# Kernel tuning notes

Hardware: AMD Instinct MI355X
Metric: run time of the kernel (lower is better)

The kernel has to match this reference:

```python
import jax, jax.numpy as jnp
import numpy as np

L = 1024; B = 64; K = 5; C = 128; R = 32; E = 64
NL = 6; NV = 2; NF = NL - NV; NC = 4; POOL = 2


def conv1d(x, w, b, dil=1):
    # x: [B, Cin, L], w: [Cout, Cin, k] -> [B, Cout, L], 'same' padding
    y = jax.lax.conv_general_dilated(x, w, (1,), 'SAME', rhs_dilation=(dil,),
                                     dimension_numbers=('NCH', 'OIH', 'NCH'))
    return y + b[None, :, None]


def block(x, w1, b1, w2, b2, dil):
    h = jax.nn.relu(conv1d(x, w1, b1, dil))
    return jax.nn.relu(conv1d(h, w2, b2))


def setup_inputs() -> dict:
    key = jax.random.key(0)
    ks = iter(jax.random.split(key, 40))
    def p(shape, scale=0.05):
        return jax.random.normal(next(ks), shape, jnp.float32) * scale
    sig = jax.random.normal(next(ks), (B, L), jnp.float32)
    ids = jax.random.randint(next(ks), (B,), 0, NC).astype(jnp.float32)
    x = jnp.concatenate([sig, ids[:, None]], axis=1)  # [B, L+1], last col = combination id
    return dict(
        x=x,
        enc0_w1=p((C, 1, K)), enc0_b1=p((C,)), enc0_w2=p((R, C, 1)), enc0_b2=p((R,)),
        enc_w1=p((NL - 1, C, R, K)), enc_b1=p((NL - 1, C)),
        enc_w2=p((NL - 1, R, C, 1)), enc_b2=p((NL - 1, R)),
        comp_w=p((E, R * NL, 1)), comp_b=p((E,)),
        decf0_w1=p((C, E, K)), decf0_b1=p((C,)), decf0_w2=p((R, C, 1)), decf0_b2=p((R,)),
        decf_w1=p((NF - 1, C, R, K)), decf_b1=p((NF - 1, C)),
        decf_w2=p((NF - 1, R, C, 1)), decf_b2=p((NF - 1, R)),
        decv_w1=p((NC, NV, C, R, K)), decv_b1=p((NC, NV, C)),
        decv_w2=p((NC, NV, R, C, 1)), decv_b2=p((NC, NV, R)),
        decv_cw=p((NC, 1, R * NL, 1)), decv_cb=p((NC, 1)),
    )


def reference(x, enc0_w1, enc0_b1, enc0_w2, enc0_b2, enc_w1, enc_b1, enc_w2, enc_b2,
              comp_w, comp_b, decf0_w1, decf0_b1, decf0_w2, decf0_b2,
              decf_w1, decf_b1, decf_w2, decf_b2,
              decv_w1, decv_b1, decv_w2, decv_b2, decv_cw, decv_cb):
    ids = jax.lax.stop_gradient(x[:, L]).astype(jnp.int32)  # combination id per sample
    h = x[:, :L][:, None, :]  # [B, 1, L]
    # --- encoder: 6 dilated blocks, concat all features ---
    feats = []
    h = block(h, enc0_w1, enc0_b1, enc0_w2, enc0_b2, 1)
    feats.append(h)
    for j in range(1, NL):
        h = block(h, enc_w1[j - 1], enc_b1[j - 1], enc_w2[j - 1], enc_b2[j - 1], 2 ** j)
        feats.append(h)
    enc = conv1d(jnp.concatenate(feats, axis=1), comp_w, comp_b)  # [B, E, L]
    enc = enc.reshape(B, E, L // POOL, POOL).mean(-1)  # AvgPool1d(POOL)
    # nearest-neighbor interpolate back to L (exact integer upscale)
    h = jnp.repeat(enc, POOL, axis=-1)
    # --- fixed decoder blocks ---
    dec = []
    h = block(h, decf0_w1, decf0_b1, decf0_w2, decf0_b2, 2 ** (NL - 1))
    dec.append(h)
    for j in range(1, NF):
        h = block(h, decf_w1[j - 1], decf_b1[j - 1], decf_w2[j - 1], decf_b2[j - 1], 2 ** (NL - 1 - j))
        dec.append(h)
    # --- per-combination variable decoder (dense dispatch + mask select) ---
    y = jnp.zeros((B, 1, L), x.dtype)
    for c in range(NC):
        hc = h
        dc = list(dec)
        for j in range(NV):
            hc = block(hc, decv_w1[c, j], decv_b1[c, j], decv_w2[c, j], decv_b2[c, j], 2 ** (NV - 1 - j))
            dc.append(hc)
        out_c = conv1d(jnp.concatenate(dc, axis=1), decv_cw[c], decv_cb[c])  # [B, 1, L]
        y = y + jnp.where((ids == c)[:, None, None], out_c, 0.0)
    return y[:, 0, :]  # [B, L]
```

## Files before the change

### kernel.cpp

```cpp
#include <hip/hip_runtime.h>
#include <hip/hip_bf16.h>

typedef unsigned short u16;
typedef short s8v __attribute__((ext_vector_type(8)));
typedef float f4v __attribute__((ext_vector_type(4)));


struct Ptrs { const float* p[25]; };

enum : int { ACT_PLANE = 2359296 };

__host__ __device__ inline int w1_off16(int l) {
  if (l == 0) return 0;
  if (l <= 5) return 4096 + (l - 1) * 20480;
  if (l == 6) return 106496;
  if (l <= 9) return 147456 + (l - 7) * 20480;
  return 208896 + (l - 10) * 20480;
}

enum : int {
  OFF_W1H = 0,
  OFF_W1L = 186368,
  OFF_W2H = 372736,
  OFF_W2L = 409600,
  OFF_CWT = 446464,
  OFF_B1  = 458752,
  OFF_B2  = 461056,
  OFF_CB  = 461632,
  OFF_VCW = 461696,
  OFF_VCB = 462464,
  OFF_PACC = 524288,
  OFF_FACC = 2621440,
  OFF_ACT0 = 2752512,
  OFF_ACT1 = 5111808,
};

__device__ __host__ inline int w1_cin(int l) { return l == 0 ? 1 : (l == 6 ? 64 : 32); }

__device__ inline const float* w1_src(const Ptrs& in, int l) {
  if (l == 0) return in.p[1];
  if (l <= 5) return in.p[5] + (l - 1) * 20480;
  if (l == 6) return in.p[11];
  if (l <= 9) return in.p[15] + (l - 7) * 20480;
  return in.p[19] + (l - 10) * 20480;
}
__device__ inline const float* w2_src(const Ptrs& in, int l) {
  if (l == 0) return in.p[3];
  if (l <= 5) return in.p[7] + (l - 1) * 4096;
  if (l == 6) return in.p[13];
  if (l <= 9) return in.p[17] + (l - 7) * 4096;
  return in.p[21] + (l - 10) * 4096;
}
__device__ inline const float* b1_src(const Ptrs& in, int l) {
  if (l == 0) return in.p[2];
  if (l <= 5) return in.p[6] + (l - 1) * 128;
  if (l == 6) return in.p[12];
  if (l <= 9) return in.p[16] + (l - 7) * 128;
  return in.p[20] + (l - 10) * 128;
}
__device__ inline const float* b2_src(const Ptrs& in, int l) {
  if (l == 0) return in.p[4];
  if (l <= 5) return in.p[8] + (l - 1) * 32;
  if (l == 6) return in.p[14];
  if (l <= 9) return in.p[18] + (l - 7) * 32;
  return in.p[22] + (l - 10) * 32;
}

__device__ inline u16 f2b(float v) {
  unsigned b = __float_as_uint(v);
  b += 0x7FFFu + ((b >> 16) & 1u);
  return (u16)(b >> 16);
}
__device__ inline float b2fl(u16 h) { return __uint_as_float((unsigned)h << 16); }
__device__ inline void splitf(float v, u16& h, u16& l) {
  h = f2b(v);
  l = f2b(v - b2fl(h));
}

__global__ __launch_bounds__(256) void prep_k(Ptrs in, float* __restrict__ ws) {
  const int job = blockIdx.x;
  const int sl = blockIdx.y;
  const int t = threadIdx.x;
  u16* w1h = (u16*)(ws + OFF_W1H);
  u16* w1l = (u16*)(ws + OFF_W1L);
  u16* w2h = (u16*)(ws + OFF_W2H);
  u16* w2l = (u16*)(ws + OFF_W2L);
  u16* cwH = (u16*)(ws + OFF_CWT);
  u16* cwL = cwH + 12288;
  if (job == 0) {
    if (sl == 0) {
      const float* src = w1_src(in, 0);
      for (int i = t; i < 4096; i += 256) {
        const int co = i >> 5, q = i & 31;
        const float v = (q < 5) ? src[co * 5 + q] : 0.f;
        u16 hh, ll; splitf(v, hh, ll);
        w1h[i] = hh; w1l[i] = ll;
      }
    }
  } else if (job < 18) {
    const int cin = w1_cin(job);
    const int lc = (cin == 64) ? 6 : 5;
    const float* src = w1_src(in, job);
    u16* dh = w1h + w1_off16(job);
    u16* dl = w1l + w1_off16(job);
    const int n = 5 * 128 * cin;
    for (int i = t + sl * 256; i < n; i += 2048) {
      const int tap = i >> (7 + lc);
      const int co = (i >> lc) & 127;
      const int ci = i & (cin - 1);
      u16 hh, ll; splitf(src[(co * cin + ci) * 5 + tap], hh, ll);
      dh[i] = hh; dl[i] = ll;
    }
  } else if (job < 36) {
    const int l = job - 18;
    const float* src = w2_src(in, l);
    for (int i = t + sl * 256; i < 4096; i += 2048) {
      u16 hh, ll; splitf(src[i], hh, ll);
      w2h[l * 4096 + i] = hh; w2l[l * 4096 + i] = ll;
    }
  } else if (job == 36) {
    const float* src = in.p[9];
    for (int i = t + sl * 256; i < 12288; i += 2048) {
      u16 hh, ll; splitf(src[i], hh, ll);
      cwH[i] = hh; cwL[i] = ll;
    }
  } else if (job == 37) {
    if (sl == 0) {
      for (int i = t; i < 18 * 128; i += 256) {
        const int l = i >> 7, r = i & 127;
        ws[OFF_B1 + i] = b1_src(in, l)[r];
      }
      for (int i = t; i < 18 * 32; i += 256) {
        const int l = i >> 5, r = i & 31;
        ws[OFF_B2 + i] = b2_src(in, l)[r];
      }
      for (int i = t; i < 64; i += 256) ws[OFF_CB + i] = in.p[10][i];
      for (int i = t; i < 768; i += 256) ws[OFF_VCW + i] = in.p[23][i];
      for (int i = t; i < 4; i += 256) ws[OFF_VCB + i] = in.p[24][i];
    }
  } else {
    u16* A = (u16*)(ws + (job == 38 ? OFF_ACT0 : OFF_ACT1));
    const uint4 z = make_uint4(0, 0, 0, 0);
    for (int i = t; i < 8192; i += 256) {
      const int cid = sl * 8192 + i;
      const int p = cid >> 15;
      const int r = cid & 32767;
      const int b = r >> 9;
      const int r2 = r & 511;
      const int pc = r2 >> 2;
      const int slot = r2 & 3;
      const int col = (pc < 64) ? pc : (1024 + pc);
      *(uint4*)&A[p * ACT_PLANE + (b * 1152 + col) * 32 + slot * 8] = z;
    }
  }
}

template <int CIN, int S, bool VAR, int EPI>
__global__ __launch_bounds__(256, 4) void blk_k(
    const void* __restrict__ src,
    const u16* __restrict__ w1h, const u16* __restrict__ w1l,
    const u16* __restrict__ w2h, const u16* __restrict__ w2l,
    const float* __restrict__ b1f, const float* __restrict__ b2f,
    u16* __restrict__ outH, int dil,
    const float* __restrict__ x, int jvar, int jf,
    const u16* __restrict__ cwtbH, const u16* __restrict__ cwtbL,
    const float* __restrict__ cb, float* __restrict__ pacc,
    const float* __restrict__ vcw, const float* __restrict__ vcb,
    float* __restrict__ facc, float* __restrict__ fout) {
  constexpr int HS = 136;
  __shared__ __align__(16) u16 lds[2 * 64 * HS];
  u16* hH = lds;
  u16* hL = lds + 64 * HS;

  const int tid = threadIdx.x;
  const int lane = tid & 63;
  const int wid = __builtin_amdgcn_readfirstlane(tid >> 6);
  const int l15 = lane & 15;
  const int g = lane >> 4;
  const int col0 = blockIdx.x * 64;
  const int b = blockIdx.y;

  if (VAR) {
    int c = (int)x[b * 1025 + 1024];
    c = c < 0 ? 0 : (c > 3 ? 3 : c);
    c = __builtin_amdgcn_readfirstlane(c);
    const int lo_ = c * 2 + jvar;
    w1h += lo_ * 20480; w1l += lo_ * 20480;
    w2h += lo_ * 4096;  w2l += lo_ * 4096;
    b1f += lo_ * 128;   b2f += lo_ * 32;
  }

  const int co0 = wid * 32;
  const f4v zf = {0.f, 0.f, 0.f, 0.f};
  const s8v z8 = {0, 0, 0, 0, 0, 0, 0, 0};
  f4v acc[2][4];
#pragma unroll
  for (int rt = 0; rt < 2; ++rt)
#pragma unroll
    for (int ct = 0; ct < 4; ++ct) acc[rt][ct] = zf;

  if (S == 1) {
    const u16* aH = (const u16*)src;
    const int gbase = (b * 1152 + col0) * 32;
#pragma unroll
    for (int k = 0; k < 3; ++k) {
      const int c2 = tid + k * 256;
      const int q = c2 >> 2, slot = c2 & 3;
      const uint4 v = *(const uint4*)(aH + gbase + c2 * 8);
      *(uint4*)&lds[q * 32 + ((slot ^ (q & 3)) << 3)] = v;
    }
#pragma unroll
    for (int k = 0; k < 3; ++k) {
      const int c2 = tid + k * 256;
      const int q = c2 >> 2, slot = c2 & 3;
      const uint4 v = *(const uint4*)(aH + ACT_PLANE + gbase + c2 * 8);
      *(uint4*)&lds[6144 + q * 32 + ((slot ^ (q & 3)) << 3)] = v;
    }
    __syncthreads();

#pragma unroll
    for (int tap = 0; tap < 5; ++tap) {
      s8v ah[2], al[2];
#pragma unroll
      for (int rt = 0; rt < 2; ++rt) {
        const int row = co0 + rt * 16 + l15;
        ah[rt] = *(const s8v*)(w1h + (tap * 128 + row) * 32 + 8 * g);
        al[rt] = *(const s8v*)(w1l + (tap * 128 + row) * 32 + 8 * g);
      }
#pragma unroll
      for (int ct = 0; ct < 4; ++ct) {
        const int q = ct * 16 + l15 + (tap - 2) * dil + 64;
        const int off = q * 32 + ((g ^ (q & 3)) << 3);
        const s8v bh = *(const s8v*)&lds[off];
        const s8v bl = *(const s8v*)&lds[6144 + off];
#pragma unroll
        for (int rt = 0; rt < 2; ++rt) {
          acc[rt][ct] = __builtin_amdgcn_mfma_f32_16x16x32_bf16(ah[rt], bh, acc[rt][ct], 0, 0, 0);
          acc[rt][ct] = __builtin_amdgcn_mfma_f32_16x16x32_bf16(ah[rt], bl, acc[rt][ct], 0, 0, 0);
          acc[rt][ct] = __builtin_amdgcn_mfma_f32_16x16x32_bf16(al[rt], bh, acc[rt][ct], 0, 0, 0);
        }
      }
    }
    __syncthreads();
  } else if (S == 0) {
    s8v ah[2], al[2];
#pragma unroll
    for (int rt = 0; rt < 2; ++rt) {
      const int row = co0 + rt * 16 + l15;
      ah[rt] = *(const s8v*)(w1h + row * 32 + 8 * g);
      al[rt] = *(const s8v*)(w1l + row * 32 + 8 * g);
    }
    const float* xf = (const float*)src;
#pragma unroll
    for (int ct = 0; ct < 4; ++ct) {
      s8v bh = z8, bl = z8;
#pragma unroll
      for (int j = 0; j < 8; ++j) {
        const int q = 8 * g + j;
        const int m = col0 + ct * 16 + l15 + (q - 2);
        float v = (q < 5 && (unsigned)m < 1024u) ? xf[b * 1025 + m] : 0.f;
        u16 hh, ll; splitf(v, hh, ll);
        bh[j] = (short)hh; bl[j] = (short)ll;
      }
#pragma unroll
      for (int rt = 0; rt < 2; ++rt) {
        acc[rt][ct] = __builtin_amdgcn_mfma_f32_16x16x32_bf16(ah[rt], bh, acc[rt][ct], 0, 0, 0);
        acc[rt][ct] = __builtin_amdgcn_mfma_f32_16x16x32_bf16(ah[rt], bl, acc[rt][ct], 0, 0, 0);
        acc[rt][ct] = __builtin_amdgcn_mfma_f32_16x16x32_bf16(al[rt], bh, acc[rt][ct], 0, 0, 0);
      }
    }
  } else {
    const float* pc = (const float*)src;
#pragma unroll
    for (int tap = 0; tap < 5; ++tap) {
#pragma unroll
      for (int ch = 0; ch < 2; ++ch) {
        s8v ah[2], al[2];
#pragma unroll
        for (int rt = 0; rt < 2; ++rt) {
          const int row = co0 + rt * 16 + l15;
          ah[rt] = *(const s8v*)(w1h + (tap * 128 + row) * 64 + ch * 32 + 8 * g);
          al[rt] = *(const s8v*)(w1l + (tap * 128 + row) * 64 + ch * 32 + 8 * g);
        }
#pragma unroll
        for (int ct = 0; ct < 4; ++ct) {
          const int m = col0 + ct * 16 + l15 + (tap - 2) * dil;
          s8v bh = z8, bl = z8;
          if ((unsigned)m < 1024u) {
            const int pcol = m >> 1;
#pragma unroll
            for (int j = 0; j < 8; ++j) {
              const float v = pc[b * 32768 + (ch * 32 + 8 * g + j) * 512 + pcol];
              u16 hh, ll; splitf(v, hh, ll);
              bh[j] = (short)hh; bl[j] = (short)ll;
            }
          }
#pragma unroll
          for (int rt = 0; rt < 2; ++rt) {
            acc[rt][ct] = __builtin_amdgcn_mfma_f32_16x16x32_bf16(ah[rt], bh, acc[rt][ct], 0, 0, 0);
            acc[rt][ct] = __builtin_amdgcn_mfma_f32_16x16x32_bf16(ah[rt], bl, acc[rt][ct], 0, 0, 0);
            acc[rt][ct] = __builtin_amdgcn_mfma_f32_16x16x32_bf16(al[rt], bh, acc[rt][ct], 0, 0, 0);
          }
        }
      }
    }
  }

#pragma unroll
  for (int rt = 0; rt < 2; ++rt) {
#pragma unroll
    for (int ct = 0; ct < 4; ++ct) {
      const int colw = ct * 16 + l15;
      unsigned ph0 = 0, ph1 = 0, pl0 = 0, pl1 = 0;
#pragma unroll
      for (int reg = 0; reg < 4; ++reg) {
        const int c2 = co0 + rt * 16 + 4 * g + reg;
        const float hv = fmaxf(acc[rt][ct][reg] + b1f[c2], 0.f);
        u16 hh, ll; splitf(hv, hh, ll);
        if (reg == 0)      { ph0 = hh;                  pl0 = ll; }
        else if (reg == 1) { ph0 |= (unsigned)hh << 16; pl0 |= (unsigned)ll << 16; }
        else if (reg == 2) { ph1 = hh;                  pl1 = ll; }
        else               { ph1 |= (unsigned)hh << 16; pl1 |= (unsigned)ll << 16; }
      }
      const int base = colw * HS + co0 + rt * 16 + 4 * g;
      *(uint2*)&hH[base] = make_uint2(ph0, ph1);
      *(uint2*)&hL[base] = make_uint2(pl0, pl1);
    }
  }
  __syncthreads();

  f4v acc2[2];
  acc2[0] = zf; acc2[1] = zf;
  const int colw2 = wid * 16 + l15;
#pragma unroll
  for (int ks = 0; ks < 4; ++ks) {
    const int k0 = ks * 32 + 8 * g;
    const s8v bh = *(const s8v*)&hH[colw2 * HS + k0];
    const s8v bl = *(const s8v*)&hL[colw2 * HS + k0];
#pragma unroll
    for (int rt = 0; rt < 2; ++rt) {
      const int row = rt * 16 + l15;
      const s8v ah2 = *(const s8v*)(w2h + row * 128 + k0);
      const s8v al2 = *(const s8v*)(w2l + row * 128 + k0);
      acc2[rt] = __builtin_amdgcn_mfma_f32_16x16x32_bf16(ah2, bh, acc2[rt], 0, 0, 0);
      acc2[rt] = __builtin_amdgcn_mfma_f32_16x16x32_bf16(ah2, bl, acc2[rt], 0, 0, 0);
      acc2[rt] = __builtin_amdgcn_mfma_f32_16x16x32_bf16(al2, bh, acc2[rt], 0, 0, 0);
    }
  }

  u16* outL = outH + ACT_PLANE;
  float vv[8];
#pragma unroll
  for (int rt = 0; rt < 2; ++rt) {
    unsigned ph0 = 0, ph1 = 0, pl0 = 0, pl1 = 0;
#pragma unroll
    for (int reg = 0; reg < 4; ++reg) {
      const int r = rt * 16 + 4 * g + reg;
      const float v = fmaxf(acc2[rt][reg] + b2f[r], 0.f);
      vv[rt * 4 + reg] = v;
      u16 hh, ll; splitf(v, hh, ll);
      if (reg == 0)      { ph0 = hh;                  pl0 = ll; }
      else if (reg == 1) { ph0 |= (unsigned)hh << 16; pl0 |= (unsigned)ll << 16; }
      else if (reg == 2) { ph1 = hh;                  pl1 = ll; }
      else               { ph1 |= (unsigned)hh << 16; pl1 |= (unsigned)ll << 16; }
    }
    if (EPI != 5) {
      const int ob = (b * 1152 + 64 + col0 + colw2) * 32 + rt * 16 + 4 * g;
      *(uint2*)&outH[ob] = make_uint2(ph0, ph1);
      *(uint2*)&outL[ob] = make_uint2(pl0, pl1);
    }
  }
  __syncthreads();

  if (EPI <= 2) {
    u16* spH = lds;
    u16* spL = lds + 1280;
    float vx[8];
#pragma unroll
    for (int i = 0; i < 8; ++i) vx[i] = __shfl_xor(vv[i], 1);
    if (!(l15 & 1)) {
      const int pl = colw2 >> 1;
#pragma unroll
      for (int i = 0; i < 8; ++i) {
        const int rt = i >> 2, reg = i & 3;
        const int r = rt * 16 + 4 * g + reg;
        const float pv = 0.5f * (vv[i] + vx[i]);
        u16 hh, ll; splitf(pv, hh, ll);
        spH[pl * 40 + r] = hh; spL[pl * 40 + r] = ll;
      }
    }
    __syncthreads();
    const u16* cwH = cwtbH + jf * 32;
    const u16* cwL = cwtbL + jf * 32;
    const s8v aH = *(const s8v*)(cwH + (wid * 16 + l15) * 192 + 8 * g);
    const s8v aL = *(const s8v*)(cwL + (wid * 16 + l15) * 192 + 8 * g);
#pragma unroll
    for (int pt = 0; pt < 2; ++pt) {
      const s8v bH = *(const s8v*)(spH + (pt * 16 + l15) * 40 + 8 * g);
      const s8v bL = *(const s8v*)(spL + (pt * 16 + l15) * 40 + 8 * g);
      f4v p = zf;
      p = __builtin_amdgcn_mfma_f32_16x16x32_bf16(aH, bH, p, 0, 0, 0);
      p = __builtin_amdgcn_mfma_f32_16x16x32_bf16(aH, bL, p, 0, 0, 0);
      p = __builtin_amdgcn_mfma_f32_16x16x32_bf16(aL, bH, p, 0, 0, 0);
#pragma unroll
      for (int reg = 0; reg < 4; ++reg) {
        const int e = wid * 16 + 4 * g + reg;
        const int pg = (col0 >> 1) + pt * 16 + l15;
        float* dst = pacc + b * 32768 + e * 512 + pg;
        const float old = (EPI == 1) ? cb[e] : *dst;
        *dst = old + p[reg];
      }
    }
  } else {
    float* ft = (float*)lds;
#pragma unroll
    for (int i = 0; i < 8; ++i) {
      const int rt = i >> 2, reg = i & 3;
      const int r = rt * 16 + 4 * g + reg;
      ft[r * 64 + colw2] = vv[i];
    }
    __syncthreads();
    if (wid == 0) {
      int c = (int)x[b * 1025 + 1024];
      c = c < 0 ? 0 : (c > 3 ? 3 : c);
      c = __builtin_amdgcn_readfirstlane(c);
      const float* w = vcw + c * 192 + jf * 32;
      float a = 0.f;
#pragma unroll
      for (int r = 0; r < 32; ++r) a = fmaf(w[r], ft[r * 64 + lane], a);
      float* fd = facc + b * 1024 + col0 + lane;
      a += (EPI == 3) ? vcb[c] : *fd;
      if (EPI == 5) fout[b * 1024 + col0 + lane] = a;
      else          *fd = a;
    }
  }
}

extern "C" void kernel_launch(void* const* d_in, const int* in_sizes, int n_in,
                              void* d_out, int out_size, void* d_ws, size_t ws_size,
                              hipStream_t stream) {
  (void)in_sizes; (void)n_in; (void)out_size; (void)ws_size;
  Ptrs P;
  for (int i = 0; i < 25; ++i) P.p[i] = (const float*)d_in[i];
  const float* x = (const float*)d_in[0];
  float* ws = (float*)d_ws;
  float* pacc = ws + OFF_PACC;
  float* facc = ws + OFF_FACC;
  u16* A0 = (u16*)(ws + OFF_ACT0);
  u16* A1 = (u16*)(ws + OFF_ACT1);
  auto W1H = [&](int l) { return (const u16*)(ws + OFF_W1H) + w1_off16(l); };
  auto W1L = [&](int l) { return (const u16*)(ws + OFF_W1L) + w1_off16(l); };
  auto W2H = [&](int l) { return (const u16*)(ws + OFF_W2H) + l * 4096; };
  auto W2L = [&](int l) { return (const u16*)(ws + OFF_W2L) + l * 4096; };
  auto BB1 = [&](int l) { return (const float*)(ws + OFF_B1) + l * 128; };
  auto BB2 = [&](int l) { return (const float*)(ws + OFF_B2) + l * 32; };
  const u16* cwtbH = (const u16*)(ws + OFF_CWT);
  const u16* cwtbL = cwtbH + 12288;
  const float* cb = ws + OFF_CB;
  const float* vcw = ws + OFF_VCW;
  const float* vcb = ws + OFF_VCB;
  float* outp = (float*)d_out;

  prep_k<<<dim3(40, 8), dim3(256), 0, stream>>>(P, ws);

  const dim3 bg(16, 64), bt(256);

  blk_k<1, 0, false, 1><<<bg, bt, 0, stream>>>(x, W1H(0), W1L(0), W2H(0), W2L(0),
      BB1(0), BB2(0), A0, 1, x, 0, 0, cwtbH, cwtbL, cb, pacc, vcw, vcb, facc, outp);
  u16* cur = A0; u16* nxt = A1;
  for (int j = 1; j <= 5; ++j) {
    blk_k<32, 1, false, 2><<<bg, bt, 0, stream>>>(cur, W1H(j), W1L(j), W2H(j), W2L(j),
        BB1(j), BB2(j), nxt, 1 << j, x, 0, j, cwtbH, cwtbL, cb, pacc, vcw, vcb, facc, outp);
    u16* t = cur; cur = nxt; nxt = t;
  }
  blk_k<64, 2, false, 3><<<bg, bt, 0, stream>>>(pacc, W1H(6), W1L(6), W2H(6), W2L(6),
      BB1(6), BB2(6), A0, 32, x, 0, 0, cwtbH, cwtbL, cb, pacc, vcw, vcb, facc, outp);
  cur = A0; nxt = A1;
  for (int j = 1; j <= 3; ++j) {
    blk_k<32, 1, false, 4><<<bg, bt, 0, stream>>>(cur, W1H(6 + j), W1L(6 + j), W2H(6 + j),
        W2L(6 + j), BB1(6 + j), BB2(6 + j), nxt, 1 << (5 - j), x, 0, j,
        cwtbH, cwtbL, cb, pacc, vcw, vcb, facc, outp);
    u16* t = cur; cur = nxt; nxt = t;
  }
  blk_k<32, 1, true, 4><<<bg, bt, 0, stream>>>(cur, W1H(10), W1L(10), W2H(10), W2L(10),
      BB1(10), BB2(10), nxt, 2, x, 0, 4, cwtbH, cwtbL, cb, pacc, vcw, vcb, facc, outp);
  { u16* t = cur; cur = nxt; nxt = t; }
  blk_k<32, 1, true, 5><<<bg, bt, 0, stream>>>(cur, W1H(10), W1L(10), W2H(10), W2L(10),
      BB1(10), BB2(10), nxt, 1, x, 1, 5, cwtbH, cwtbL, cb, pacc, vcw, vcb, facc, outp);
}
```

Baseline: 400.5 us.

## Fuse all layer launches into one persistent cooperative kernel with grid syncs

Replaces the prep kernel and the twelve per-layer launches with a single cooperative mega-kernel. Blocks loop over 1024 tiles per layer and separate layers with grid.sync(). The goal is to remove launch gaps and tail effects between small kernels. In exchange, the epilogue selector becomes a runtime value instead of a template constant, which may add branching and register pressure. Grid-wide barriers can also cost more than kernel boundaries.

```diff
diff --git a/kernel.cpp b/kernel.cpp
--- a/kernel.cpp
+++ b/kernel.cpp
@@ -1,5 +1,8 @@
 #include <hip/hip_runtime.h>
 #include <hip/hip_bf16.h>
+#include <hip/hip_cooperative_groups.h>
+
+namespace cg = cooperative_groups;
 
 typedef unsigned short u16;
 typedef short s8v __attribute__((ext_vector_type(8)));
@@ -77,10 +80,7 @@
   l = f2b(v - b2fl(h));
 }
 
-__global__ __launch_bounds__(256) void prep_k(Ptrs in, float* __restrict__ ws) {
-  const int job = blockIdx.x;
-  const int sl = blockIdx.y;
-  const int t = threadIdx.x;
+__device__ void prep_body(int job, int sl, int t, const Ptrs& in, float* __restrict__ ws) {
   u16* w1h = (u16*)(ws + OFF_W1H);
   u16* w1l = (u16*)(ws + OFF_W1L);
   u16* w2h = (u16*)(ws + OFF_W2H);
@@ -155,20 +155,20 @@
   }
 }
 
-template <int CIN, int S, bool VAR, int EPI>
-__global__ __launch_bounds__(256, 4) void blk_k(
-    const void* __restrict__ src,
+template <int CIN, int S, bool VAR>
+__device__ void layer_body(
+    int tile, const void* __restrict__ src,
     const u16* __restrict__ w1h, const u16* __restrict__ w1l,
     const u16* __restrict__ w2h, const u16* __restrict__ w2l,
     const float* __restrict__ b1f, const float* __restrict__ b2f,
     u16* __restrict__ outH, int dil,
-    const float* __restrict__ x, int jvar, int jf,
+    const float* __restrict__ x, int jvar, int jf, int epi,
     const u16* __restrict__ cwtbH, const u16* __restrict__ cwtbL,
     const float* __restrict__ cb, float* __restrict__ pacc,
     const float* __restrict__ vcw, const float* __restrict__ vcb,
-    float* __restrict__ facc, float* __restrict__ fout) {
+    float* __restrict__ facc, float* __restrict__ fout,
+    u16* lds) {
   constexpr int HS = 136;
-  __shared__ __align__(16) u16 lds[2 * 64 * HS];
   u16* hH = lds;
   u16* hL = lds + 64 * HS;
 
@@ -177,8 +177,10 @@
   const int wid = __builtin_amdgcn_readfirstlane(tid >> 6);
   const int l15 = lane & 15;
   const int g = lane >> 4;
-  const int col0 = blockIdx.x * 64;
-  const int b = blockIdx.y;
+  const int col0 = (tile & 15) * 64;
+  const int b = tile >> 4;
+
+  __syncthreads();
 
   if (VAR) {
     int c = (int)x[b * 1025 + 1024];
@@ -364,7 +366,7 @@
       else if (reg == 2) { ph1 = hh;                  pl1 = ll; }
       else               { ph1 |= (unsigned)hh << 16; pl1 |= (unsigned)ll << 16; }
     }
-    if (EPI != 5) {
+    if (epi != 5) {
       const int ob = (b * 1152 + 64 + col0 + colw2) * 32 + rt * 16 + 4 * g;
       *(uint2*)&outH[ob] = make_uint2(ph0, ph1);
       *(uint2*)&outL[ob] = make_uint2(pl0, pl1);
@@ -372,7 +374,7 @@
   }
   __syncthreads();
 
-  if (EPI <= 2) {
+  if (epi <= 2) {
     u16* spH = lds;
     u16* spL = lds + 1280;
     float vx[8];
@@ -407,7 +409,7 @@
         const int e = wid * 16 + 4 * g + reg;
         const int pg = (col0 >> 1) + pt * 16 + l15;
         float* dst = pacc + b * 32768 + e * 512 + pg;
-        const float old = (EPI == 1) ? cb[e] : *dst;
+        const float old = (epi == 1) ? cb[e] : *dst;
         *dst = old + p[reg];
       }
     }
@@ -429,11 +431,86 @@
 #pragma unroll
       for (int r = 0; r < 32; ++r) a = fmaf(w[r], ft[r * 64 + lane], a);
       float* fd = facc + b * 1024 + col0 + lane;
-      a += (EPI == 3) ? vcb[c] : *fd;
-      if (EPI == 5) fout[b * 1024 + col0 + lane] = a;
+      a += (epi == 3) ? vcb[c] : *fd;
+      if (epi == 5) fout[b * 1024 + col0 + lane] = a;
       else          *fd = a;
     }
   }
+}
+
+__global__ __launch_bounds__(256, 4) void mega_k(Ptrs in, float* __restrict__ ws,
+                                                 float* __restrict__ outp) {
+  __shared__ __align__(16) u16 lds[2 * 64 * 136];
+  cg::grid_group grid = cg::this_grid();
+  const float* x = in.p[0];
+  float* pacc = ws + OFF_PACC;
+  float* facc = ws + OFF_FACC;
+  u16* A0 = (u16*)(ws + OFF_ACT0);
+  u16* A1 = (u16*)(ws + OFF_ACT1);
+  const u16* w1hb = (const u16*)(ws + OFF_W1H);
+  const u16* w1lb = (const u16*)(ws + OFF_W1L);
+  const u16* w2hb = (const u16*)(ws + OFF_W2H);
+  const u16* w2lb = (const u16*)(ws + OFF_W2L);
+  const u16* cwtbH = (const u16*)(ws + OFF_CWT);
+  const u16* cwtbL = cwtbH + 12288;
+  const float* b1b = ws + OFF_B1;
+  const float* b2b = ws + OFF_B2;
+  const float* cb = ws + OFF_CB;
+  const float* vcw = ws + OFF_VCW;
+  const float* vcb = ws + OFF_VCB;
+
+  for (int w = blockIdx.x; w < 320; w += gridDim.x)
+    prep_body(w >> 3, w & 7, threadIdx.x, in, ws);
+  grid.sync();
+
+  for (int t = blockIdx.x; t < 1024; t += gridDim.x)
+    layer_body<1, 0, false>(t, x, w1hb + w1_off16(0), w1lb + w1_off16(0),
+        w2hb, w2lb, b1b, b2b, A0, 1, x, 0, 0, 1,
+        cwtbH, cwtbL, cb, pacc, vcw, vcb, facc, outp, lds);
+  grid.sync();
+
+  u16* cur = A0; u16* nxt = A1;
+  for (int j = 1; j <= 5; ++j) {
+    for (int t = blockIdx.x; t < 1024; t += gridDim.x)
+      layer_body<32, 1, false>(t, cur, w1hb + w1_off16(j), w1lb + w1_off16(j),
+          w2hb + j * 4096, w2lb + j * 4096, b1b + j * 128, b2b + j * 32,
+          nxt, 1 << j, x, 0, j, 2,
+          cwtbH, cwtbL, cb, pacc, vcw, vcb, facc, outp, lds);
+    grid.sync();
+    u16* tmp = cur; cur = nxt; nxt = tmp;
+  }
+
+  for (int t = blockIdx.x; t < 1024; t += gridDim.x)
+    layer_body<64, 2, false>(t, pacc, w1hb + w1_off16(6), w1lb + w1_off16(6),
+        w2hb + 6 * 4096, w2lb + 6 * 4096, b1b + 6 * 128, b2b + 6 * 32,
+        A0, 32, x, 0, 0, 3,
+        cwtbH, cwtbL, cb, pacc, vcw, vcb, facc, outp, lds);
+  grid.sync();
+
+  cur = A0; nxt = A1;
+  for (int j = 1; j <= 3; ++j) {
+    for (int t = blockIdx.x; t < 1024; t += gridDim.x)
+      layer_body<32, 1, false>(t, cur, w1hb + w1_off16(6 + j), w1lb + w1_off16(6 + j),
+          w2hb + (6 + j) * 4096, w2lb + (6 + j) * 4096,
+          b1b + (6 + j) * 128, b2b + (6 + j) * 32,
+          nxt, 1 << (5 - j), x, 0, j, 4,
+          cwtbH, cwtbL, cb, pacc, vcw, vcb, facc, outp, lds);
+    grid.sync();
+    u16* tmp = cur; cur = nxt; nxt = tmp;
+  }
+
+  for (int t = blockIdx.x; t < 1024; t += gridDim.x)
+    layer_body<32, 1, true>(t, cur, w1hb + w1_off16(10), w1lb + w1_off16(10),
+        w2hb + 10 * 4096, w2lb + 10 * 4096, b1b + 10 * 128, b2b + 10 * 32,
+        nxt, 2, x, 0, 4, 4,
+        cwtbH, cwtbL, cb, pacc, vcw, vcb, facc, outp, lds);
+  grid.sync();
+  { u16* tmp = cur; cur = nxt; nxt = tmp; }
+  for (int t = blockIdx.x; t < 1024; t += gridDim.x)
+    layer_body<32, 1, true>(t, cur, w1hb + w1_off16(10), w1lb + w1_off16(10),
+        w2hb + 10 * 4096, w2lb + 10 * 4096, b1b + 10 * 128, b2b + 10 * 32,
+        nxt, 1, x, 1, 5, 5,
+        cwtbH, cwtbL, cb, pacc, vcw, vcb, facc, outp, lds);
 }
 
 extern "C" void kernel_launch(void* const* d_in, const int* in_sizes, int n_in,
@@ -442,49 +519,17 @@
   (void)in_sizes; (void)n_in; (void)out_size; (void)ws_size;
   Ptrs P;
   for (int i = 0; i < 25; ++i) P.p[i] = (const float*)d_in[i];
-  const float* x = (const float*)d_in[0];
   float* ws = (float*)d_ws;
-  float* pacc = ws + OFF_PACC;
-  float* facc = ws + OFF_FACC;
-  u16* A0 = (u16*)(ws + OFF_ACT0);
-  u16* A1 = (u16*)(ws + OFF_ACT1);
-  auto W1H = [&](int l) { return (const u16*)(ws + OFF_W1H) + w1_off16(l); };
-  auto W1L = [&](int l) { return (const u16*)(ws + OFF_W1L) + w1_off16(l); };
-  auto W2H = [&](int l) { return (const u16*)(ws + OFF_W2H) + l * 4096; };
-  auto W2L = [&](int l) { return (const u16*)(ws + OFF_W2L) + l * 4096; };
-  auto BB1 = [&](int l) { return (const float*)(ws + OFF_B1) + l * 128; };
-  auto BB2 = [&](int l) { return (const float*)(ws + OFF_B2) + l * 32; };
-  const u16* cwtbH = (const u16*)(ws + OFF_CWT);
-  const u16* cwtbL = cwtbH + 12288;
-  const float* cb = ws + OFF_CB;
-  const float* vcw = ws + OFF_VCW;
-  const float* vcb = ws + OFF_VCB;
   float* outp = (float*)d_out;
 
-  prep_k<<<dim3(40, 8), dim3(256), 0, stream>>>(P, ws);
-
-  const dim3 bg(16, 64), bt(256);
-
-  blk_k<1, 0, false, 1><<<bg, bt, 0, stream>>>(x, W1H(0), W1L(0), W2H(0), W2L(0),
-      BB1(0), BB2(0), A0, 1, x, 0, 0, cwtbH, cwtbL, cb, pacc, vcw, vcb, facc, outp);
-  u16* cur = A0; u16* nxt = A1;
-  for (int j = 1; j <= 5; ++j) {
-    blk_k<32, 1, false, 2><<<bg, bt, 0, stream>>>(cur, W1H(j), W1L(j), W2H(j), W2L(j),
-        BB1(j), BB2(j), nxt, 1 << j, x, 0, j, cwtbH, cwtbL, cb, pacc, vcw, vcb, facc, outp);
-    u16* t = cur; cur = nxt; nxt = t;
-  }
-  blk_k<64, 2, false, 3><<<bg, bt, 0, stream>>>(pacc, W1H(6), W1L(6), W2H(6), W2L(6),
-      BB1(6), BB2(6), A0, 32, x, 0, 0, cwtbH, cwtbL, cb, pacc, vcw, vcb, facc, outp);
-  cur = A0; nxt = A1;
-  for (int j = 1; j <= 3; ++j) {
-    blk_k<32, 1, false, 4><<<bg, bt, 0, stream>>>(cur, W1H(6 + j), W1L(6 + j), W2H(6 + j),
-        W2L(6 + j), BB1(6 + j), BB2(6 + j), nxt, 1 << (5 - j), x, 0, j,
-        cwtbH, cwtbL, cb, pacc, vcw, vcb, facc, outp);
-    u16* t = cur; cur = nxt; nxt = t;
-  }
-  blk_k<32, 1, true, 4><<<bg, bt, 0, stream>>>(cur, W1H(10), W1L(10), W2H(10), W2L(10),
-      BB1(10), BB2(10), nxt, 2, x, 0, 4, cwtbH, cwtbL, cb, pacc, vcw, vcb, facc, outp);
-  { u16* t = cur; cur = nxt; nxt = t; }
-  blk_k<32, 1, true, 5><<<bg, bt, 0, stream>>>(cur, W1H(10), W1L(10), W2H(10), W2L(10),
-      BB1(10), BB2(10), nxt, 1, x, 1, 5, cwtbH, cwtbL, cb, pacc, vcw, vcb, facc, outp);
-}
+  int nCU = 256;
+  hipDeviceGetAttribute(&nCU, hipDeviceAttributeMultiprocessorCount, 0);
+  int perCU = 0;
+  hipOccupancyMaxActiveBlocksPerMultiprocessor(&perCU, mega_k, 256, 0);
+  if (perCU < 1) perCU = 1;
+  long grid = (long)perCU * nCU;
+  if (grid > 1024) grid = 1024;
+
+  void* kargs[] = {(void*)&P, (void*)&ws, (void*)&outp};
+  hipLaunchCooperativeKernel(mega_k, dim3((unsigned)grid), dim3(256), kargs, 0, stream);
+}
```

After: 1.200 ms. 3x slower.

## Stage pooled encoder features in swizzled LDS and transpose pacc layout

Applied to the files above, without the earlier changes.

Changes the pooled accumulator pacc from channel-major to position-major [b][pcol][e], so epilogue writes become 16-byte vector stores and the decoder-input loads become coalesced. The decoder's first conv now pre-stages a window of pooled columns into LDS as bf16 hi/lo pairs once, instead of gathering and splitting scalars from global memory for every tap and tile. The padded LDS hidden buffer is replaced with an XOR-swizzled 128-stride layout to avoid bank conflicts, and launch bounds are raised to 5 blocks per SM. The cost is extra barriers and a staging loop, and occupancy depends on register pressure.

```diff
diff --git a/kernel.cpp b/kernel.cpp
--- a/kernel.cpp
+++ b/kernel.cpp
@@ -156,7 +156,7 @@
 }
 
 template <int CIN, int S, bool VAR, int EPI>
-__global__ __launch_bounds__(256, 4) void blk_k(
+__global__ __launch_bounds__(256, 5) void blk_k(
     const void* __restrict__ src,
     const u16* __restrict__ w1h, const u16* __restrict__ w1l,
     const u16* __restrict__ w2h, const u16* __restrict__ w2l,
@@ -167,10 +167,9 @@
     const float* __restrict__ cb, float* __restrict__ pacc,
     const float* __restrict__ vcw, const float* __restrict__ vcb,
     float* __restrict__ facc, float* __restrict__ fout) {
-  constexpr int HS = 136;
-  __shared__ __align__(16) u16 lds[2 * 64 * HS];
+  __shared__ __align__(16) u16 lds[16384];
   u16* hH = lds;
-  u16* hL = lds + 64 * HS;
+  u16* hL = lds + 8192;
 
   const int tid = threadIdx.x;
   const int lane = tid & 63;
@@ -271,6 +270,19 @@
     }
   } else {
     const float* pc = (const float*)src;
+    const int p0 = col0 >> 1;
+#pragma unroll
+    for (int k = 0; k < 24; ++k) {
+      const int idx = tid + k * 256;
+      const int s = idx >> 6, e = idx & 63;
+      const int pcol = p0 - 32 + s;
+      const float v = ((unsigned)pcol < 512u) ? pc[b * 32768 + pcol * 64 + e] : 0.f;
+      u16 hh, ll; splitf(v, hh, ll);
+      const int off = s * 64 + (e ^ ((s & 7) << 3));
+      lds[off] = hh; lds[6144 + off] = ll;
+    }
+    __syncthreads();
+
 #pragma unroll
     for (int tap = 0; tap < 5; ++tap) {
 #pragma unroll
@@ -285,16 +297,10 @@
 #pragma unroll
         for (int ct = 0; ct < 4; ++ct) {
           const int m = col0 + ct * 16 + l15 + (tap - 2) * dil;
-          s8v bh = z8, bl = z8;
-          if ((unsigned)m < 1024u) {
-            const int pcol = m >> 1;
-#pragma unroll
-            for (int j = 0; j < 8; ++j) {
-              const float v = pc[b * 32768 + (ch * 32 + 8 * g + j) * 512 + pcol];
-              u16 hh, ll; splitf(v, hh, ll);
-              bh[j] = (short)hh; bl[j] = (short)ll;
-            }
-          }
+          const int sIdx = (m >> 1) - p0 + 32;
+          const int off = sIdx * 64 + ((ch * 32 + 8 * g) ^ ((sIdx & 7) << 3));
+          const s8v bh = *(const s8v*)&lds[off];
+          const s8v bl = *(const s8v*)&lds[6144 + off];
 #pragma unroll
           for (int rt = 0; rt < 2; ++rt) {
             acc[rt][ct] = __builtin_amdgcn_mfma_f32_16x16x32_bf16(ah[rt], bh, acc[rt][ct], 0, 0, 0);
@@ -304,6 +310,7 @@
         }
       }
     }
+    __syncthreads();
   }
 
 #pragma unroll
@@ -322,7 +329,7 @@
         else if (reg == 2) { ph1 = hh;                  pl1 = ll; }
         else               { ph1 |= (unsigned)hh << 16; pl1 |= (unsigned)ll << 16; }
       }
-      const int base = colw * HS + co0 + rt * 16 + 4 * g;
+      const int base = colw * 128 + ((co0 + rt * 16 + 4 * g) ^ ((colw & 7) << 3));
       *(uint2*)&hH[base] = make_uint2(ph0, ph1);
       *(uint2*)&hL[base] = make_uint2(pl0, pl1);
     }
@@ -335,8 +342,9 @@
 #pragma unroll
   for (int ks = 0; ks < 4; ++ks) {
     const int k0 = ks * 32 + 8 * g;
-    const s8v bh = *(const s8v*)&hH[colw2 * HS + k0];
-    const s8v bl = *(const s8v*)&hL[colw2 * HS + k0];
+    const int off2 = colw2 * 128 + (k0 ^ ((colw2 & 7) << 3));
+    const s8v bh = *(const s8v*)&hH[off2];
+    const s8v bl = *(const s8v*)&hL[off2];
 #pragma unroll
     for (int rt = 0; rt < 2; ++rt) {
       const int row = rt * 16 + l15;
@@ -402,14 +410,18 @@
       p = __builtin_amdgcn_mfma_f32_16x16x32_bf16(aH, bH, p, 0, 0, 0);
       p = __builtin_amdgcn_mfma_f32_16x16x32_bf16(aH, bL, p, 0, 0, 0);
       p = __builtin_amdgcn_mfma_f32_16x16x32_bf16(aL, bH, p, 0, 0, 0);
-#pragma unroll
-      for (int reg = 0; reg < 4; ++reg) {
-        const int e = wid * 16 + 4 * g + reg;
-        const int pg = (col0 >> 1) + pt * 16 + l15;
-        float* dst = pacc + b * 32768 + e * 512 + pg;
-        const float old = (EPI == 1) ? cb[e] : *dst;
-        *dst = old + p[reg];
-      }
+      const int e0 = wid * 16 + 4 * g;
+      const int pg = (col0 >> 1) + pt * 16 + l15;
+      float* dst = pacc + b * 32768 + pg * 64 + e0;
+      f4v old;
+      if (EPI == 1) {
+        old[0] = cb[e0]; old[1] = cb[e0 + 1]; old[2] = cb[e0 + 2]; old[3] = cb[e0 + 3];
+      } else {
+        old = *(const f4v*)dst;
+      }
+#pragma unroll
+      for (int reg = 0; reg < 4; ++reg) p[reg] += old[reg];
+      *(f4v*)dst = p;
     }
   } else {
     float* ft = (float*)lds;
```

After: 371.0 us. 7.4% less time.
